# Optimization experiments

Hardware: AMD Instinct MI355X
Metric: run time of the kernel (lower is better)

Reference implementation:

```python
import jax, jax.numpy as jnp
import numpy as np
from math import sqrt

B, S, E, H = 4, 4096, 512, 64


def setup_inputs() -> dict:
    key = jax.random.key(0)
    ks = jax.random.split(key, 9)
    std = sqrt(2.0 / (E + 4 * H))
    x_query = jax.random.normal(ks[0], (B, S, E), dtype=jnp.float32)
    x_key = jax.random.normal(ks[1], (B, S, E), dtype=jnp.float32)
    x_value = jax.random.normal(ks[2], (B, S, E), dtype=jnp.float32)
    Wq = jax.random.normal(ks[3], (E, H), dtype=jnp.float32) * std
    Wk = jax.random.normal(ks[4], (E, H), dtype=jnp.float32) * std
    Wv = jax.random.normal(ks[5], (E, H), dtype=jnp.float32) * std
    bq = jnp.zeros((H,), dtype=jnp.float32)
    bk = jnp.zeros((H,), dtype=jnp.float32)
    bv = jnp.zeros((H,), dtype=jnp.float32)
    # causal mask: True entries are masked out (set to -inf), as in scores[mask] = -inf
    mask = jnp.broadcast_to(jnp.triu(jnp.ones((S, S), dtype=bool), k=1), (B, S, S))
    return {"x_query": x_query, "x_key": x_key, "x_value": x_value,
            "Wq": Wq, "bq": bq, "Wk": Wk, "bk": bk, "Wv": Wv, "bv": bv,
            "mask": mask}


def reference(x_query, x_key, x_value, Wq, bq, Wk, bk, Wv, bv, mask):
    scale = 1.0 / sqrt(H)
    Q = x_query @ Wq + bq              # [B, S, H]
    K = x_key @ Wk + bk                # [B, S, H]
    V = x_value @ Wv + bv              # [B, S, H]
    scores = jnp.einsum('bqh,bkh->bqk', Q, K) * scale  # [B, S, S]
    scores = jnp.where(mask, -jnp.inf, scores)
    attn = jax.nn.softmax(scores, axis=-1)
    Z = jnp.einsum('bqk,bkh->bqh', attn, V)             # [B, S, H]
    return Z
```

## Files before the change

### kernel.cpp

```cpp
#include <hip/hip_runtime.h>
#include <math.h>

#define BB 4
#define SS 4096
#define EE 512
#define HH 64
#define NSPLIT 8
#define NQ (BB * SS)

typedef _Float16 f16x8 __attribute__((ext_vector_type(8)));
typedef short    s16x8 __attribute__((ext_vector_type(8)));
typedef float    f32x4 __attribute__((ext_vector_type(4)));

static __device__ __forceinline__ unsigned short f2h(float f) {
    _Float16 h = (_Float16)f;
    return __builtin_bit_cast(unsigned short, h);
}

static __device__ __forceinline__ f32x4 mfma_f16(s16x8 a, s16x8 b, f32x4 c) {
    return __builtin_amdgcn_mfma_f32_16x16x32_f16(
        __builtin_bit_cast(f16x8, a), __builtin_bit_cast(f16x8, b), c, 0, 0, 0);
}

__global__ __launch_bounds__(256) void wprep_kernel(
    const float* __restrict__ Wq, const float* __restrict__ Wk,
    const float* __restrict__ Wv, unsigned short* __restrict__ WT)
{
    const int mat = blockIdx.y;
    const float* W = (mat == 0) ? Wq : ((mat == 1) ? Wk : Wv);
    const int base = blockIdx.x * 2048;
    for (int ii = threadIdx.x; ii < 2048; ii += 256) {
        const int i = base + ii;
        const int k = i >> 6, n = i & 63;
        WT[((size_t)mat * HH + n) * EE + k] = f2h(W[i]);
    }
}

__global__ __launch_bounds__(256) void qkv_proj_kernel(
    const float* __restrict__ Xq, const float* __restrict__ Xk, const float* __restrict__ Xv,
    const float* __restrict__ bq, const float* __restrict__ bk, const float* __restrict__ bv,
    const unsigned short* __restrict__ WT,
    unsigned short* __restrict__ Qf, unsigned short* __restrict__ Kf,
    unsigned short* __restrict__ Vt)
{
    const int mtx = blockIdx.y;
    const float* X    = (mtx == 0) ? Xq : ((mtx == 1) ? Xk : Xv);
    const float* bias = (mtx == 0) ? bq : ((mtx == 1) ? bk : bv);

    __shared__ unsigned short As[64 * 72];
    __shared__ unsigned short Bs[64 * 72];

    const int tid  = threadIdx.x;
    const int lane = tid & 63;
    const int w    = tid >> 6;
    const int l15  = lane & 15;
    const int lg   = lane >> 4;
    const int r0   = blockIdx.x * 64;

    const int arow = tid >> 2;
    const int asg  = tid & 3;

    f32x4 acc[4] = {{0,0,0,0},{0,0,0,0},{0,0,0,0},{0,0,0,0}};

    for (int c = 0; c < EE / 64; ++c) {
        const float* xp = &X[(size_t)(r0 + arow) * EE + c * 64 + asg * 16];
        const float4 x0 = ((const float4*)xp)[0];
        const float4 x1 = ((const float4*)xp)[1];
        const float4 x2 = ((const float4*)xp)[2];
        const float4 x3 = ((const float4*)xp)[3];
        const size_t wb = ((size_t)mtx * HH + arow) * EE + c * 64 + asg * 16;
        const s16x8 w0 = *(const s16x8*)&WT[wb];
        const s16x8 w1 = *(const s16x8*)&WT[wb + 8];
        __syncthreads();

        const float xs[16] = {x0.x,x0.y,x0.z,x0.w, x1.x,x1.y,x1.z,x1.w,
                              x2.x,x2.y,x2.z,x2.w, x3.x,x3.y,x3.z,x3.w};
        s16x8 a0, a1;
        #pragma unroll
        for (int i = 0; i < 8; ++i) {
            a0[i] = (short)f2h(xs[i]);
            a1[i] = (short)f2h(xs[8 + i]);
        }
        *(s16x8*)&As[arow * 72 + asg * 16]     = a0;
        *(s16x8*)&As[arow * 72 + asg * 16 + 8] = a1;
        *(s16x8*)&Bs[arow * 72 + asg * 16]     = w0;
        *(s16x8*)&Bs[arow * 72 + asg * 16 + 8] = w1;
        __syncthreads();

        const int ma = (w * 16 + l15) * 72;
        const s16x8 af0 = *(const s16x8*)&As[ma + lg * 8];
        const s16x8 af1 = *(const s16x8*)&As[ma + 32 + lg * 8];
        #pragma unroll
        for (int f = 0; f < 4; ++f) {
            const int nb = (f * 16 + l15) * 72;
            const s16x8 bf0 = *(const s16x8*)&Bs[nb + lg * 8];
            const s16x8 bf1 = *(const s16x8*)&Bs[nb + 32 + lg * 8];
            acc[f] = mfma_f16(af0, bf0, acc[f]);
            acc[f] = mfma_f16(af1, bf1, acc[f]);
        }
    }

    float bcol[4];
    #pragma unroll
    for (int f = 0; f < 4; ++f) bcol[f] = bias[f * 16 + l15];
    const float qs = (mtx == 0) ? 0.125f : 1.0f;

    if (mtx < 2) {
        unsigned short* Out = (mtx == 0) ? Qf : Kf;
        #pragma unroll
        for (int f = 0; f < 4; ++f)
            #pragma unroll
            for (int r = 0; r < 4; ++r)
                Out[(size_t)(r0 + w * 16 + lg * 4 + r) * HH + f * 16 + l15] =
                    f2h((acc[f][r] + bcol[f]) * qs);
    } else {
        const int b  = r0 >> 12;
        const int s0 = (r0 & 4095) + w * 16 + lg * 4;
        #pragma unroll
        for (int f = 0; f < 4; ++f) {
            ushort4 pk;
            pk.x = f2h(acc[f][0] + bcol[f]);
            pk.y = f2h(acc[f][1] + bcol[f]);
            pk.z = f2h(acc[f][2] + bcol[f]);
            pk.w = f2h(acc[f][3] + bcol[f]);
            *(ushort4*)&Vt[((size_t)b * HH + f * 16 + l15) * SS + s0] = pk;
        }
    }
}

__global__ __launch_bounds__(256) void attn_partial_kernel(
    const unsigned short* __restrict__ Qf, const unsigned short* __restrict__ Kf,
    const unsigned short* __restrict__ Vt, float* __restrict__ o_part,
    float* __restrict__ m_part, float* __restrict__ l_part)
{
    __shared__ unsigned short Ks[2][64 * 68];
    __shared__ unsigned short Vs[2][64 * 68];
    __shared__ unsigned short Pl[4 * 16 * 68];

    const int tid  = threadIdx.x;
    const int b    = blockIdx.z;
    const int cch  = blockIdx.y;
    const int qb0  = blockIdx.x * 64;
    const int lane = tid & 63;
    const int w    = tid >> 6;
    const int l15  = lane & 15;
    const int lg   = lane >> 4;
    const int qw0  = qb0 + w * 16;

    const size_t qrow = (size_t)(b * SS + qw0 + l15) * HH;
    const s16x8 qf0 = *(const s16x8*)&Qf[qrow + lg * 8];
    const s16x8 qf1 = *(const s16x8*)&Qf[qrow + 32 + lg * 8];

    f32x4 o[4] = {{0,0,0,0},{0,0,0,0},{0,0,0,0},{0,0,0,0}};
    float m[4], l[4];
    #pragma unroll
    for (int r = 0; r < 4; ++r) { m[r] = -1.0e30f; l[r] = 0.f; }

    const int kkey = tid >> 2, ksg = tid & 3;
    const unsigned short* Kb = Kf + (size_t)b * SS * HH;
    const unsigned short* Vb = Vt + (size_t)b * HH * SS;

    const int T   = blockIdx.x + 1;
    const int tpc = (T + NSPLIT - 1) / NSPLIT;
    const int t0  = cch * tpc;
    const int t1  = min(t0 + tpc, T);
    const int nt  = t1 - t0;
    unsigned short* PW = Pl + w * (16 * 68);

    s16x8 ka, kb2, va, vb2;

    if (nt > 0) {
        const int k0 = t0 * 64;
        ka  = *(const s16x8*)&Kb[(size_t)(k0 + kkey) * HH + ksg * 8];
        kb2 = *(const s16x8*)&Kb[(size_t)(k0 + kkey) * HH + 32 + ksg * 8];
        va  = *(const s16x8*)&Vb[(size_t)kkey * SS + k0 + ksg * 8];
        vb2 = *(const s16x8*)&Vb[(size_t)kkey * SS + k0 + 32 + ksg * 8];
        *(s16x8*)&Ks[0][kkey * 68 + ksg * 8]      = ka;
        *(s16x8*)&Ks[0][kkey * 68 + 32 + ksg * 8] = kb2;
        *(s16x8*)&Vs[0][kkey * 68 + ksg * 8]      = va;
        *(s16x8*)&Vs[0][kkey * 68 + 32 + ksg * 8] = vb2;
        __syncthreads();
    }

    for (int i = 0; i < nt; ++i) {
        const int t   = t0 + i;
        const int cur = i & 1;
        const int k0  = t * 64;

        if (i + 1 < nt) {
            const int kn = (t + 1) * 64;
            ka  = *(const s16x8*)&Kb[(size_t)(kn + kkey) * HH + ksg * 8];
            kb2 = *(const s16x8*)&Kb[(size_t)(kn + kkey) * HH + 32 + ksg * 8];
            va  = *(const s16x8*)&Vb[(size_t)kkey * SS + kn + ksg * 8];
            vb2 = *(const s16x8*)&Vb[(size_t)kkey * SS + kn + 32 + ksg * 8];
        }

        f32x4 sc[4];
        #pragma unroll
        for (int f = 0; f < 4; ++f) {
            const int kr = (f * 16 + l15) * 68;
            const s16x8 kfa = *(const s16x8*)&Ks[cur][kr + lg * 8];
            const s16x8 kfb = *(const s16x8*)&Ks[cur][kr + 32 + lg * 8];
            f32x4 z = {0, 0, 0, 0};
            z = mfma_f16(qf0, kfa, z);
            z = mfma_f16(qf1, kfb, z);
            sc[f] = z;
        }

        float sv[4][4];
        #pragma unroll
        for (int f = 0; f < 4; ++f)
            #pragma unroll
            for (int r = 0; r < 4; ++r) sv[f][r] = sc[f][r];
        if (k0 + 63 > qw0) {
            #pragma unroll
            for (int f = 0; f < 4; ++f)
                #pragma unroll
                for (int r = 0; r < 4; ++r) {
                    const int qr = qw0 + lg * 4 + r;
                    if (k0 + f * 16 + l15 > qr) sv[f][r] = -3.0e38f;
                }
        }

        float tm[4];
        #pragma unroll
        for (int r = 0; r < 4; ++r)
            tm[r] = fmaxf(fmaxf(sv[0][r], sv[1][r]), fmaxf(sv[2][r], sv[3][r]));
        #pragma unroll
        for (int d = 1; d < 16; d <<= 1)
            #pragma unroll
            for (int r = 0; r < 4; ++r) tm[r] = fmaxf(tm[r], __shfl_xor(tm[r], d));

        bool grow = false;
        #pragma unroll
        for (int r = 0; r < 4; ++r) grow = grow || (tm[r] > m[r] + 8.0f);
        if (__any((int)grow)) {
            #pragma unroll
            for (int r = 0; r < 4; ++r) {
                const float mn = fmaxf(m[r], tm[r]);
                const float al = __expf(m[r] - mn);
                m[r] = mn;
                l[r] *= al;
                #pragma unroll
                for (int f = 0; f < 4; ++f) o[f][r] *= al;
            }
        }

        float p[4][4];
        #pragma unroll
        for (int f = 0; f < 4; ++f)
            #pragma unroll
            for (int r = 0; r < 4; ++r) p[f][r] = __expf(sv[f][r] - m[r]);
        #pragma unroll
        for (int r = 0; r < 4; ++r)
            l[r] += p[0][r] + p[1][r] + p[2][r] + p[3][r];

        #pragma unroll
        for (int f = 0; f < 4; ++f)
            #pragma unroll
            for (int r = 0; r < 4; ++r)
                PW[(lg * 4 + r) * 68 + f * 16 + l15] = f2h(p[f][r]);
        const s16x8 pa0 = *(const s16x8*)&PW[l15 * 68 + lg * 8];
        const s16x8 pa1 = *(const s16x8*)&PW[l15 * 68 + 32 + lg * 8];
        #pragma unroll
        for (int f = 0; f < 4; ++f) {
            const int vr = (f * 16 + l15) * 68;
            const s16x8 vfa = *(const s16x8*)&Vs[cur][vr + lg * 8];
            const s16x8 vfb = *(const s16x8*)&Vs[cur][vr + 32 + lg * 8];
            o[f] = mfma_f16(pa0, vfa, o[f]);
            o[f] = mfma_f16(pa1, vfb, o[f]);
        }

        if (i + 1 < nt) {
            const int nxt = cur ^ 1;
            *(s16x8*)&Ks[nxt][kkey * 68 + ksg * 8]      = ka;
            *(s16x8*)&Ks[nxt][kkey * 68 + 32 + ksg * 8] = kb2;
            *(s16x8*)&Vs[nxt][kkey * 68 + ksg * 8]      = va;
            *(s16x8*)&Vs[nxt][kkey * 68 + 32 + ksg * 8] = vb2;
            __syncthreads();
        }
    }

    #pragma unroll
    for (int d = 1; d < 16; d <<= 1)
        #pragma unroll
        for (int r = 0; r < 4; ++r) l[r] += __shfl_xor(l[r], d);

    #pragma unroll
    for (int r = 0; r < 4; ++r) {
        const size_t qlin = (size_t)b * SS + qb0 + w * 16 + lg * 4 + r;
        float* Op = o_part + ((size_t)cch * NQ + qlin) * HH;
        #pragma unroll
        for (int f = 0; f < 4; ++f) Op[f * 16 + l15] = o[f][r];
        if (l15 == 0) {
            m_part[(size_t)cch * NQ + qlin] = m[r];
            l_part[(size_t)cch * NQ + qlin] = l[r];
        }
    }
}

__global__ __launch_bounds__(256) void attn_combine_kernel(
    const float* __restrict__ o_part, const float* __restrict__ m_part,
    const float* __restrict__ l_part, float* __restrict__ O)
{
    const int g = blockIdx.x * 256 + threadIdx.x;
    const size_t qlin = (size_t)(g >> 4);
    const int h0 = (g & 15) * 4;

    float mv[NSPLIT], lv[NSPLIT];
    float M = -INFINITY;
    #pragma unroll
    for (int cc = 0; cc < NSPLIT; ++cc) {
        mv[cc] = m_part[(size_t)cc * NQ + qlin];
        lv[cc] = l_part[(size_t)cc * NQ + qlin];
        M = fmaxf(M, mv[cc]);
    }
    float L = 0.f;
    float4 acc = make_float4(0.f, 0.f, 0.f, 0.f);
    #pragma unroll
    for (int cc = 0; cc < NSPLIT; ++cc) {
        const float wc = __expf(mv[cc] - M);
        L += lv[cc] * wc;
        const float4 oc = *(const float4*)&o_part[((size_t)cc * NQ + qlin) * HH + h0];
        acc.x += wc * oc.x; acc.y += wc * oc.y;
        acc.z += wc * oc.z; acc.w += wc * oc.w;
    }
    const float inv = 1.0f / L;
    acc.x *= inv; acc.y *= inv; acc.z *= inv; acc.w *= inv;
    *(float4*)&O[qlin * HH + h0] = acc;
}

extern "C" void kernel_launch(void* const* d_in, const int* in_sizes, int n_in,
                              void* d_out, int out_size, void* d_ws, size_t ws_size,
                              hipStream_t stream) {
    const float* xq = (const float*)d_in[0];
    const float* xk = (const float*)d_in[1];
    const float* xv = (const float*)d_in[2];
    const float* Wq = (const float*)d_in[3];
    const float* bq = (const float*)d_in[4];
    const float* Wk = (const float*)d_in[5];
    const float* bk = (const float*)d_in[6];
    const float* Wv = (const float*)d_in[7];
    const float* bv = (const float*)d_in[8];

    unsigned short* Qf = (unsigned short*)d_ws;
    unsigned short* Kf = Qf + (size_t)NQ * HH;
    unsigned short* Vt = Kf + (size_t)NQ * HH;
    unsigned short* WT = Vt + (size_t)NQ * HH;
    float* o_part = (float*)(WT + (size_t)3 * HH * EE);
    float* m_part = o_part + (size_t)NSPLIT * NQ * HH;
    float* l_part = m_part + (size_t)NSPLIT * NQ;

    wprep_kernel<<<dim3(16, 3), 256, 0, stream>>>(Wq, Wk, Wv, WT);

    qkv_proj_kernel<<<dim3(NQ / 64, 3), 256, 0, stream>>>(
        xq, xk, xv, bq, bk, bv, WT, Qf, Kf, Vt);

    attn_partial_kernel<<<dim3(SS / 64, NSPLIT, BB), 256, 0, stream>>>(
        Qf, Kf, Vt, o_part, m_part, l_part);

    attn_combine_kernel<<<(NQ * 16) / 256, 256, 0, stream>>>(
        o_part, m_part, l_part, (float*)d_out);
}
```

Before: 439.7 us.

## Fold log2e into Q scale, use exp2, single-buffer K/V LDS, halve KV splits

Q is pre-scaled by 0.125·log2(e), so softmax exponentials become exp2f with no extra multiply, and the rescale threshold is adjusted to match. The K/V shared buffers drop from double to single buffering, with an extra barrier before each overwrite, which halves LDS use and may raise occupancy but serializes loads against compute. The number of key splits drops from 8 to 4, cutting partial-result traffic and combine work while launching fewer blocks.

```diff
diff --git a/kernel.cpp b/kernel.cpp
--- a/kernel.cpp
+++ b/kernel.cpp
@@ -5,7 +5,7 @@
 #define SS 4096
 #define EE 512
 #define HH 64
-#define NSPLIT 8
+#define NSPLIT 4
 #define NQ (BB * SS)
 
 typedef _Float16 f16x8 __attribute__((ext_vector_type(8)));
@@ -103,7 +103,7 @@
     float bcol[4];
     #pragma unroll
     for (int f = 0; f < 4; ++f) bcol[f] = bias[f * 16 + l15];
-    const float qs = (mtx == 0) ? 0.125f : 1.0f;
+    const float qs = (mtx == 0) ? 0.18033688f : 1.0f;
 
     if (mtx < 2) {
         unsigned short* Out = (mtx == 0) ? Qf : Kf;
@@ -133,8 +133,8 @@
     const unsigned short* __restrict__ Vt, float* __restrict__ o_part,
     float* __restrict__ m_part, float* __restrict__ l_part)
 {
-    __shared__ unsigned short Ks[2][64 * 68];
-    __shared__ unsigned short Vs[2][64 * 68];
+    __shared__ unsigned short Ks[64 * 68];
+    __shared__ unsigned short Vs[64 * 68];
     __shared__ unsigned short Pl[4 * 16 * 68];
 
     const int tid  = threadIdx.x;
@@ -175,17 +175,16 @@
         kb2 = *(const s16x8*)&Kb[(size_t)(k0 + kkey) * HH + 32 + ksg * 8];
         va  = *(const s16x8*)&Vb[(size_t)kkey * SS + k0 + ksg * 8];
         vb2 = *(const s16x8*)&Vb[(size_t)kkey * SS + k0 + 32 + ksg * 8];
-        *(s16x8*)&Ks[0][kkey * 68 + ksg * 8]      = ka;
-        *(s16x8*)&Ks[0][kkey * 68 + 32 + ksg * 8] = kb2;
-        *(s16x8*)&Vs[0][kkey * 68 + ksg * 8]      = va;
-        *(s16x8*)&Vs[0][kkey * 68 + 32 + ksg * 8] = vb2;
+        *(s16x8*)&Ks[kkey * 68 + ksg * 8]      = ka;
+        *(s16x8*)&Ks[kkey * 68 + 32 + ksg * 8] = kb2;
+        *(s16x8*)&Vs[kkey * 68 + ksg * 8]      = va;
+        *(s16x8*)&Vs[kkey * 68 + 32 + ksg * 8] = vb2;
         __syncthreads();
     }
 
     for (int i = 0; i < nt; ++i) {
-        const int t   = t0 + i;
-        const int cur = i & 1;
-        const int k0  = t * 64;
+        const int t  = t0 + i;
+        const int k0 = t * 64;
 
         if (i + 1 < nt) {
             const int kn = (t + 1) * 64;
@@ -199,8 +198,8 @@
         #pragma unroll
         for (int f = 0; f < 4; ++f) {
             const int kr = (f * 16 + l15) * 68;
-            const s16x8 kfa = *(const s16x8*)&Ks[cur][kr + lg * 8];
-            const s16x8 kfb = *(const s16x8*)&Ks[cur][kr + 32 + lg * 8];
+            const s16x8 kfa = *(const s16x8*)&Ks[kr + lg * 8];
+            const s16x8 kfb = *(const s16x8*)&Ks[kr + 32 + lg * 8];
             f32x4 z = {0, 0, 0, 0};
             z = mfma_f16(qf0, kfa, z);
             z = mfma_f16(qf1, kfb, z);
@@ -233,12 +232,12 @@
 
         bool grow = false;
         #pragma unroll
-        for (int r = 0; r < 4; ++r) grow = grow || (tm[r] > m[r] + 8.0f);
+        for (int r = 0; r < 4; ++r) grow = grow || (tm[r] > m[r] + 11.5416f);
         if (__any((int)grow)) {
             #pragma unroll
             for (int r = 0; r < 4; ++r) {
                 const float mn = fmaxf(m[r], tm[r]);
-                const float al = __expf(m[r] - mn);
+                const float al = exp2f(m[r] - mn);
                 m[r] = mn;
                 l[r] *= al;
                 #pragma unroll
@@ -250,7 +249,7 @@
         #pragma unroll
         for (int f = 0; f < 4; ++f)
             #pragma unroll
-            for (int r = 0; r < 4; ++r) p[f][r] = __expf(sv[f][r] - m[r]);
+            for (int r = 0; r < 4; ++r) p[f][r] = exp2f(sv[f][r] - m[r]);
         #pragma unroll
         for (int r = 0; r < 4; ++r)
             l[r] += p[0][r] + p[1][r] + p[2][r] + p[3][r];
@@ -262,21 +261,22 @@
                 PW[(lg * 4 + r) * 68 + f * 16 + l15] = f2h(p[f][r]);
         const s16x8 pa0 = *(const s16x8*)&PW[l15 * 68 + lg * 8];
         const s16x8 pa1 = *(const s16x8*)&PW[l15 * 68 + 32 + lg * 8];
+
         #pragma unroll
         for (int f = 0; f < 4; ++f) {
             const int vr = (f * 16 + l15) * 68;
-            const s16x8 vfa = *(const s16x8*)&Vs[cur][vr + lg * 8];
-            const s16x8 vfb = *(const s16x8*)&Vs[cur][vr + 32 + lg * 8];
+            const s16x8 vfa = *(const s16x8*)&Vs[vr + lg * 8];
+            const s16x8 vfb = *(const s16x8*)&Vs[vr + 32 + lg * 8];
             o[f] = mfma_f16(pa0, vfa, o[f]);
             o[f] = mfma_f16(pa1, vfb, o[f]);
         }
 
         if (i + 1 < nt) {
-            const int nxt = cur ^ 1;
-            *(s16x8*)&Ks[nxt][kkey * 68 + ksg * 8]      = ka;
-            *(s16x8*)&Ks[nxt][kkey * 68 + 32 + ksg * 8] = kb2;
-            *(s16x8*)&Vs[nxt][kkey * 68 + ksg * 8]      = va;
-            *(s16x8*)&Vs[nxt][kkey * 68 + 32 + ksg * 8] = vb2;
+            __syncthreads();
+            *(s16x8*)&Ks[kkey * 68 + ksg * 8]      = ka;
+            *(s16x8*)&Ks[kkey * 68 + 32 + ksg * 8] = kb2;
+            *(s16x8*)&Vs[kkey * 68 + ksg * 8]      = va;
+            *(s16x8*)&Vs[kkey * 68 + 32 + ksg * 8] = vb2;
             __syncthreads();
         }
     }
@@ -319,7 +319,7 @@
     float4 acc = make_float4(0.f, 0.f, 0.f, 0.f);
     #pragma unroll
     for (int cc = 0; cc < NSPLIT; ++cc) {
-        const float wc = __expf(mv[cc] - M);
+        const float wc = exp2f(mv[cc] - M);
         L += lv[cc] * wc;
         const float4 oc = *(const float4*)&o_part[((size_t)cc * NQ + qlin) * HH + h0];
         acc.x += wc * oc.x; acc.y += wc * oc.y;
```

Result: no change. 446.5 us (+1.5%).
